# Performance work log

Measured on AMD Instinct MI355X. Metric: run time of the kernel, lower is better.

Reference implementation:

```python
import jax, jax.numpy as jnp
import numpy as np

LN_EPS = 1e-5


def setup_inputs() -> dict:
    key = jax.random.key(0)
    ks = jax.random.split(key, 8)
    B, S, D = 8, 2048, 1024
    scale = 1.0 / np.sqrt(D)
    return {
        "inp": jax.random.normal(ks[0], (B, S, D), dtype=jnp.float32),
        "lens": jax.random.randint(ks[1], (B,), 1, S + 1, dtype=jnp.int64),
        "Wq": jax.random.normal(ks[2], (D, D), dtype=jnp.float32) * scale,
        "bq": jnp.zeros((D,), dtype=jnp.float32),
        "Wk": jax.random.normal(ks[3], (D, D), dtype=jnp.float32) * scale,
        "bk": jnp.zeros((D,), dtype=jnp.float32),
        "Wv": jax.random.normal(ks[4], (D, D), dtype=jnp.float32) * scale,
        "bv": jnp.zeros((D,), dtype=jnp.float32),
        "ln_gamma": jnp.ones((D,), dtype=jnp.float32),
        "ln_beta": jnp.zeros((D,), dtype=jnp.float32),
    }


def reference(inp, lens, Wq, bq, Wk, bk, Wv, bv, ln_gamma, ln_beta):
    # inp: [B, S, D]; dk = dv = D
    B, S, D = inp.shape
    q = jnp.einsum("bsd,kd->bsk", inp, Wq) + bq  # [B, S, D]
    k = jnp.einsum("bsd,kd->bsk", inp, Wk) + bk
    v = jnp.einsum("bsd,kd->bsk", inp, Wv) + bv
    # scores[b, i, j] = q[b, i] . k[b, j]
    scores = jnp.einsum("bid,bjd->bij", q, k)  # [B, S, S]
    # NON-standard: softmax over the QUERY axis (dim=1), then divide by sqrt(dk)
    attn = jax.nn.softmax(scores, axis=1) / jnp.sqrt(jnp.asarray(D, scores.dtype))
    selfatt = jnp.einsum("bij,bjd->bid", attn, v)  # [B, S, D]
    # LayerNorm over last dim, then mean-pool over sequence (sum / seq_len)
    mu = jnp.mean(selfatt, axis=-1, keepdims=True)
    var = jnp.mean(jnp.square(selfatt - mu), axis=-1, keepdims=True)
    ln = (selfatt - mu) * jax.lax.rsqrt(var + LN_EPS) * ln_gamma + ln_beta
    context = jnp.sum(ln, axis=1) / S  # [B, D]
    return context
```

## Files before the change

### kernel.cpp

```cpp
#include <hip/hip_runtime.h>
#include <hip/hip_fp16.h>

#define B_ 8
#define S_ 2048
#define D_ 1024
#define M_ (B_ * S_)
#define NCH 8
#define LN_EPS 1e-5f

typedef _Float16 f16;
typedef _Float16 half8 __attribute__((ext_vector_type(8)));
typedef _Float16 half4_t __attribute__((ext_vector_type(4)));
typedef float floatx4 __attribute__((ext_vector_type(4)));

__device__ __forceinline__ void gload_lds16(const void* g, void* l) {
  __builtin_amdgcn_global_load_lds((const __attribute__((address_space(1))) void*)g,
                                   (__attribute__((address_space(3))) void*)l, 16, 0, 0);
}

__device__ __forceinline__ void xcd_remap(int& bx, int& by, int& bz) {
  const int gx = gridDim.x, gy = gridDim.y;
  const int nb = gx * gy * (int)gridDim.z;
  int f = blockIdx.x + gx * (blockIdx.y + gy * blockIdx.z);
  const int cpx = nb >> 3;
  f = (f & 7) * cpx + (f >> 3);
  bx = f % gx;
  f /= gx;
  by = f % gy;
  bz = f / gy;
}

__global__ void k_cvt(const float* __restrict__ src, f16* __restrict__ dst, int n4) {
  int stride = gridDim.x * blockDim.x;
  for (int i = blockIdx.x * blockDim.x + threadIdx.x; i < n4; i += stride) {
    float4 v = ((const float4*)src)[i];
    half4_t h;
    h.x = (f16)v.x; h.y = (f16)v.y; h.z = (f16)v.z; h.w = (f16)v.w;
    ((half4_t*)dst)[i] = h;
  }
}

__global__ void k_cvtw(const float* __restrict__ a, const float* __restrict__ b,
                       const float* __restrict__ c, f16* __restrict__ dst) {
  const int n4 = D_ * D_ / 4;
  const int i = blockIdx.x * 256 + threadIdx.x;
  const int which = i / n4, off = i - which * n4;
  const float* s = which == 0 ? a : (which == 1 ? b : c);
  const float4 v = ((const float4*)s)[off];
  half4_t h;
  h.x = (f16)v.x; h.y = (f16)v.y; h.z = (f16)v.z; h.w = (f16)v.w;
  ((half4_t*)dst)[i] = h;
}

#define STG_A(tn, h, buf)                                                     \
  {                                                                           \
    const f16* g = aG + (size_t)(tn) * 64 + (size_t)(h) * 128 * K;            \
    f16* l = As + (buf) * 16384 + (h) * 8192 + lOff;                          \
    gload_lds16(g, l);                                                        \
    gload_lds16(g + (size_t)64 * K, l + 4096);                                \
  }
#define STG_B(tn, h, buf)                                                     \
  {                                                                           \
    const f16* g = bG + (size_t)(tn) * 64 + (size_t)(h) * 128 * K;            \
    f16* l = Bs + (buf) * 16384 + (h) * 8192 + lOff;                          \
    gload_lds16(g, l);                                                        \
    gload_lds16(g + (size_t)64 * K, l + 4096);                                \
  }

__device__ __forceinline__ void gemm8_loop(
    const f16* aG, const f16* bG, f16* As, f16* Bs, const int K, const int lOff,
    const int wr, const int wc, const int fr, const int fs0, const int fs1,
    floatx4 (&acc)[2][4][2][2]) {
  const int NT = K >> 6;
  const int NP = NT >> 1;

  STG_A(0, 0, 0);
  STG_B(0, 0, 0);
  STG_B(0, 1, 0);
  STG_A(0, 1, 0);
  STG_A(1, 0, 1);
  STG_B(1, 0, 1);
  asm volatile("s_waitcnt vmcnt(4)" ::: "memory");
  __builtin_amdgcn_s_barrier();

  half8 af[4][2], bf0[2][2], bf1[2][2];

#define LDA(BUF, MH)                                                          \
  _Pragma("unroll") for (int m = 0; m < 4; ++m) {                             \
    const f16* Ac = As + (BUF) * 16384;                                       \
    const int ar = ((MH) * 128 + wr * 64 + m * 16 + fr) * 64;                 \
    af[m][0] = *(const half8*)(Ac + ar + fs0);                                \
    af[m][1] = *(const half8*)(Ac + ar + fs1);                                \
  }
#define LDB(BUF, NH, DST)                                                     \
  _Pragma("unroll") for (int n = 0; n < 2; ++n) {                             \
    const f16* Bc = Bs + (BUF) * 16384;                                       \
    const int br = ((NH) * 128 + wc * 32 + n * 16 + fr) * 64;                 \
    DST[n][0] = *(const half8*)(Bc + br + fs0);                               \
    DST[n][1] = *(const half8*)(Bc + br + fs1);                               \
  }
#define PH(LOADS, MH, NH, BF, STAGE_STMT, WAIT_STMT)                          \
  {                                                                           \
    LOADS;                                                                    \
    STAGE_STMT;                                                               \
    __builtin_amdgcn_s_barrier();                                             \
    __builtin_amdgcn_s_setprio(1);                                            \
    _Pragma("unroll") for (int m = 0; m < 4; ++m)                             \
      _Pragma("unroll") for (int n = 0; n < 2; ++n)                           \
        _Pragma("unroll") for (int kk = 0; kk < 2; ++kk)                      \
          acc[MH][m][NH][n] = __builtin_amdgcn_mfma_f32_16x16x32_f16(         \
              af[m][kk], BF[n][kk], acc[MH][m][NH][n], 0, 0, 0);              \
    __builtin_amdgcn_s_setprio(0);                                            \
    WAIT_STMT;                                                                \
    __builtin_amdgcn_s_barrier();                                             \
  }
#define VW4 asm volatile("s_waitcnt vmcnt(4)" ::: "memory")
#define VW2 asm volatile("s_waitcnt vmcnt(2)" ::: "memory")
#define VW0 asm volatile("s_waitcnt vmcnt(0)" ::: "memory")
#define NOW (void)0

  for (int p = 0; p < NP; ++p) {
    const int t0 = 2 * p;
    const bool mid = (t0 + 2 < NT);
    const bool nxt = (t0 + 3 < NT);
    const bool last = (p == NP - 1);

    PH(LDA(0, 0); LDB(0, 0, bf0), 0, 0, bf0, STG_B(t0 + 1, 1, 1), NOW);
    PH(LDB(0, 1, bf1), 0, 1, bf1, STG_A(t0 + 1, 1, 1), NOW);
    PH(LDA(0, 1), 1, 1, bf1, if (mid) STG_A(t0 + 2, 0, 0), NOW);
    PH(NOW, 1, 0, bf0, if (mid) STG_B(t0 + 2, 0, 0), VW4);
    PH(LDA(1, 0); LDB(1, 0, bf0), 0, 0, bf0, if (mid) STG_B(t0 + 2, 1, 0),
       if (last) { VW2; });
    PH(LDB(1, 1, bf1), 0, 1, bf1, if (mid) STG_A(t0 + 2, 1, 0),
       if (last) { VW0; });
    PH(LDA(1, 1), 1, 1, bf1, if (nxt) STG_A(t0 + 3, 0, 1), NOW);
    PH(NOW, 1, 0, bf0, if (nxt) STG_B(t0 + 3, 0, 1), if (!last) { VW4; });
  }
#undef PH
#undef LDA
#undef LDB
#undef VW4
#undef VW2
#undef VW0
#undef NOW
}

template <bool OUTF16, bool BIAS>
__global__ __launch_bounds__(512, 2) void k_gemm8(
    const f16* __restrict__ A, const f16* __restrict__ Bm, void* __restrict__ Cv,
    const float* __restrict__ bias, const int K, const int N,
    const long sA, const long sB, const long sC) {
  __shared__ f16 As[2 * 256 * 64];
  __shared__ f16 Bs[2 * 256 * 64];
  int bx, by, bz;
  xcd_remap(bx, by, bz);
  const int tid = threadIdx.x;
  const int wid = tid >> 6, lane = tid & 63;
  const int wr = wid >> 2, wc = wid & 3;
  const int fr = lane & 15;

  const f16* Ab = A + (size_t)bz * sA + (size_t)by * 256 * K;
  const f16* Bb = Bm + (size_t)bz * sB + (size_t)bx * 256 * K;
  const int srow = tid >> 3;
  const int sslot = (tid & 7) ^ (srow & 7);
  const f16* aG = Ab + (size_t)srow * K + sslot * 8;
  const f16* bG = Bb + (size_t)srow * K + sslot * 8;
  const int lOff = srow * 64 + (tid & 7) * 8;

  const int sx = lane & 7;
  const int fs0 = (((lane >> 4)) ^ sx) * 8;
  const int fs1 = ((4 + (lane >> 4)) ^ sx) * 8;

  floatx4 acc[2][4][2][2] = {};
  gemm8_loop(aG, bG, As, Bs, K, lOff, wr, wc, fr, fs0, fs1, acc);

#pragma unroll
  for (int mh = 0; mh < 2; ++mh)
#pragma unroll
    for (int m = 0; m < 4; ++m) {
      const int row0 = by * 256 + mh * 128 + wr * 64 + m * 16 + (lane >> 4) * 4;
#pragma unroll
      for (int nh = 0; nh < 2; ++nh)
#pragma unroll
        for (int n = 0; n < 2; ++n) {
          const int col = bx * 256 + nh * 128 + wc * 32 + n * 16 + (lane & 15);
          float bv = 0.0f;
          if constexpr (BIAS) bv = bias[col];
#pragma unroll
          for (int r = 0; r < 4; ++r) {
            const float v = acc[mh][m][nh][n][r] + bv;
            if constexpr (OUTF16)
              ((f16*)Cv)[(size_t)bz * sC + (size_t)(row0 + r) * N + col] = (f16)v;
            else
              ((float*)Cv)[(size_t)bz * sC + (size_t)(row0 + r) * N + col] = v;
          }
        }
    }
}

__global__ __launch_bounds__(512, 2) void k_qkv8b(
    const f16* __restrict__ X, const f16* __restrict__ W,
    f16* __restrict__ Qh, f16* __restrict__ Kh, f16* __restrict__ Vh,
    const float* __restrict__ bq, const float* __restrict__ bk,
    const float* __restrict__ bv) {
  __shared__ f16 As[2 * 256 * 64];
  __shared__ f16 Bs[2 * 256 * 64];
  int bx, by, bz;
  xcd_remap(bx, by, bz);
  const int K = D_;
  const int tid = threadIdx.x;
  const int wid = tid >> 6, lane = tid & 63;
  const int wr = wid >> 2, wc = wid & 3;
  const int fr = lane & 15;

  f16* outp = bz == 0 ? Qh : (bz == 1 ? Kh : Vh);
  const float* bp = bz == 0 ? bq : (bz == 1 ? bk : bv);

  const f16* Ab = X + (size_t)by * 256 * K;
  const f16* Bb = W + (size_t)bz * D_ * D_ + (size_t)bx * 256 * K;
  const int srow = tid >> 3;
  const int sslot = (tid & 7) ^ (srow & 7);
  const f16* aG = Ab + (size_t)srow * K + sslot * 8;
  const f16* bG = Bb + (size_t)srow * K + sslot * 8;
  const int lOff = srow * 64 + (tid & 7) * 8;

  const int sx = lane & 7;
  const int fs0 = (((lane >> 4)) ^ sx) * 8;
  const int fs1 = ((4 + (lane >> 4)) ^ sx) * 8;

  floatx4 acc[2][4][2][2] = {};
  gemm8_loop(aG, bG, As, Bs, K, lOff, wr, wc, fr, fs0, fs1, acc);

#pragma unroll
  for (int mh = 0; mh < 2; ++mh)
#pragma unroll
    for (int m = 0; m < 4; ++m) {
      const int row0 = by * 256 + mh * 128 + wr * 64 + m * 16 + (lane >> 4) * 4;
#pragma unroll
      for (int nh = 0; nh < 2; ++nh)
#pragma unroll
        for (int n = 0; n < 2; ++n) {
          const int col = bx * 256 + nh * 128 + wc * 32 + n * 16 + (lane & 15);
          const float bvv = bp[col];
#pragma unroll
          for (int r = 0; r < 4; ++r)
            outp[(size_t)(row0 + r) * D_ + col] = (f16)(acc[mh][m][nh][n][r] + bvv);
        }
    }
}

__global__ __launch_bounds__(512, 2) void k_scores8(
    const f16* __restrict__ Q, const f16* __restrict__ Kx, f16* __restrict__ Sc,
    float* __restrict__ pm, float* __restrict__ pz) {
  __shared__ f16 As[2 * 256 * 64];
  __shared__ f16 Bs[2 * 256 * 64];
  __shared__ float smax[2][256];
  __shared__ float ssum[2][256];
  int bx, by, bz;
  xcd_remap(bx, by, bz);
  const int tid = threadIdx.x;
  const int wid = tid >> 6, lane = tid & 63;
  const int wr = wid >> 2, wc = wid & 3;
  const int fr = lane & 15;
  const int K = D_;

  const f16* Ab = Q + (size_t)bz * S_ * D_ + (size_t)by * 256 * K;
  const f16* Bb = Kx + (size_t)bz * S_ * D_ + (size_t)bx * 256 * K;
  const int srow = tid >> 3;
  const int sslot = (tid & 7) ^ (srow & 7);
  const f16* aG = Ab + (size_t)srow * K + sslot * 8;
  const f16* bG = Bb + (size_t)srow * K + sslot * 8;
  const int lOff = srow * 64 + (tid & 7) * 8;

  const int sx = lane & 7;
  const int fs0 = (((lane >> 4)) ^ sx) * 8;
  const int fs1 = ((4 + (lane >> 4)) ^ sx) * 8;

  floatx4 acc[2][4][2][2] = {};
  gemm8_loop(aG, bG, As, Bs, K, lOff, wr, wc, fr, fs0, fs1, acc);

#pragma unroll
  for (int mh = 0; mh < 2; ++mh)
#pragma unroll
    for (int m = 0; m < 4; ++m) {
      const int row0 = by * 256 + mh * 128 + wr * 64 + m * 16 + (lane >> 4) * 4;
#pragma unroll
      for (int nh = 0; nh < 2; ++nh)
#pragma unroll
        for (int n = 0; n < 2; ++n) {
          const int col = bx * 256 + nh * 128 + wc * 32 + n * 16 + fr;
#pragma unroll
          for (int r = 0; r < 4; ++r)
            Sc[(size_t)bz * S_ * S_ + (size_t)(row0 + r) * S_ + col] =
                (f16)acc[mh][m][nh][n][r];
        }
    }

  float cmax[2][2], csum[2][2];
#pragma unroll
  for (int nh = 0; nh < 2; ++nh)
#pragma unroll
    for (int n = 0; n < 2; ++n) {
      float mx = -1e30f;
#pragma unroll
      for (int mh = 0; mh < 2; ++mh)
#pragma unroll
        for (int m = 0; m < 4; ++m)
#pragma unroll
          for (int r = 0; r < 4; ++r)
            mx = fmaxf(mx, (float)(f16)acc[mh][m][nh][n][r]);
      float zz = 0.f;
#pragma unroll
      for (int mh = 0; mh < 2; ++mh)
#pragma unroll
        for (int m = 0; m < 4; ++m)
#pragma unroll
          for (int r = 0; r < 4; ++r)
            zz += __expf((float)(f16)acc[mh][m][nh][n][r] - mx);
#pragma unroll
      for (int o = 16; o <= 32; o <<= 1) {
        const float om = __shfl_xor(mx, o);
        const float oz = __shfl_xor(zz, o);
        const float nm = fmaxf(mx, om);
        zz = zz * __expf(mx - nm) + oz * __expf(om - nm);
        mx = nm;
      }
      cmax[nh][n] = mx;
      csum[nh][n] = zz;
    }
  __syncthreads();
  if ((lane >> 4) == 0) {
#pragma unroll
    for (int nh = 0; nh < 2; ++nh)
#pragma unroll
      for (int n = 0; n < 2; ++n) {
        const int c = nh * 128 + wc * 32 + n * 16 + fr;
        smax[wr][c] = cmax[nh][n];
        ssum[wr][c] = csum[nh][n];
      }
  }
  __syncthreads();
  if (wr == 0 && (lane >> 4) == 0) {
#pragma unroll
    for (int nh = 0; nh < 2; ++nh)
#pragma unroll
      for (int n = 0; n < 2; ++n) {
        const int c = nh * 128 + wc * 32 + n * 16 + fr;
        const float m0 = smax[0][c], m1 = smax[1][c];
        const float nm = fmaxf(m0, m1);
        const float zz = ssum[0][c] * __expf(m0 - nm) + ssum[1][c] * __expf(m1 - nm);
        const size_t o = ((size_t)bz * NCH + by) * S_ + bx * 256 + c;
        pm[o] = nm;
        pz[o] = zz;
      }
  }
}

__global__ void k_combine(const float* __restrict__ pm, const float* __restrict__ pz,
                          float* __restrict__ mcol, float* __restrict__ cscale) {
  const int b = blockIdx.y;
  const int j = blockIdx.x * 256 + threadIdx.x;
  float m = -1e30f;
#pragma unroll
  for (int ch = 0; ch < NCH; ++ch) m = fmaxf(m, pm[((size_t)b * NCH + ch) * S_ + j]);
  float z = 0.f;
#pragma unroll
  for (int ch = 0; ch < NCH; ++ch)
    z += pz[((size_t)b * NCH + ch) * S_ + j] * __expf(pm[((size_t)b * NCH + ch) * S_ + j] - m);
  mcol[(size_t)b * S_ + j] = m;
  cscale[(size_t)b * S_ + j] = 1.0f / (z * 32.0f);
}

__global__ void k_pexp16(f16* __restrict__ P, const float* __restrict__ mcol,
                         const float* __restrict__ cscale) {
  const int n4 = B_ * S_ * S_ / 4;
  const int stride = gridDim.x * blockDim.x;
  for (int i = blockIdx.x * blockDim.x + threadIdx.x; i < n4; i += stride) {
    const size_t e = (size_t)i * 4;
    const int z = (int)(e / ((size_t)S_ * S_));
    const int j = (int)(e & (S_ - 1));
    const half4_t s4 = ((const half4_t*)P)[i];
    const float4 mv = *(const float4*)(mcol + (size_t)z * S_ + j);
    const float4 cv = *(const float4*)(cscale + (size_t)z * S_ + j);
    half4_t h;
    h.x = (f16)(__expf((float)s4.x - mv.x) * cv.x);
    h.y = (f16)(__expf((float)s4.y - mv.y) * cv.y);
    h.z = (f16)(__expf((float)s4.z - mv.z) * cv.z);
    h.w = (f16)(__expf((float)s4.w - mv.w) * cv.w);
    ((half4_t*)P)[i] = h;
  }
}

__global__ void k_transpose(const f16* __restrict__ V, f16* __restrict__ Vt) {
  __shared__ f16 t[64][72];
  const int b = blockIdx.z;
  const int j0 = blockIdx.x * 64, d0 = blockIdx.y * 64;
  const int rr = threadIdx.x >> 4;
  const int cc = (threadIdx.x & 15) * 4;
#pragma unroll
  for (int p = 0; p < 4; ++p) {
    const int j = rr + p * 16;
    const half4_t v = *(const half4_t*)(V + ((size_t)b * S_ + j0 + j) * D_ + d0 + cc);
    *(half4_t*)&t[j][cc] = v;
  }
  __syncthreads();
#pragma unroll
  for (int p = 0; p < 4; ++p) {
    const int d = rr + p * 16;
    half4_t v;
    v.x = t[cc][d]; v.y = t[cc + 1][d]; v.z = t[cc + 2][d]; v.w = t[cc + 3][d];
    *(half4_t*)(Vt + ((size_t)b * D_ + d0 + d) * S_ + j0 + cc) = v;
  }
}

__global__ __launch_bounds__(256) void k_ln_pool(
    const f16* __restrict__ selfatt, const float* __restrict__ gamma,
    const float* __restrict__ beta, float* __restrict__ part) {
  __shared__ float lds[4 * 1024];
  const int tid = threadIdx.x, wid = tid >> 6, lane = tid & 63;
  const int row0 = blockIdx.x * 64 + wid * 16;
  float g[16], be[16], acc[16];
#pragma unroll
  for (int t = 0; t < 16; ++t) {
    g[t] = gamma[lane + 64 * t];
    be[t] = beta[lane + 64 * t];
    acc[t] = 0.f;
  }
  for (int r = 0; r < 16; ++r) {
    const f16* xp = selfatt + (size_t)(row0 + r) * D_ + lane;
    float x[16], sum = 0.f, sq = 0.f;
#pragma unroll
    for (int t = 0; t < 16; ++t) {
      x[t] = (float)xp[64 * t];
      sum += x[t];
      sq += x[t] * x[t];
    }
#pragma unroll
    for (int o = 32; o > 0; o >>= 1) {
      sum += __shfl_xor(sum, o);
      sq += __shfl_xor(sq, o);
    }
    const float mu = sum * (1.f / 1024.f);
    const float var = sq * (1.f / 1024.f) - mu * mu;
    const float rstd = rsqrtf(var + LN_EPS);
#pragma unroll
    for (int t = 0; t < 16; ++t) acc[t] += (x[t] - mu) * rstd * g[t] + be[t];
  }
#pragma unroll
  for (int t = 0; t < 16; ++t) lds[wid * 1024 + lane + 64 * t] = acc[t];
  __syncthreads();
#pragma unroll
  for (int c = 0; c < 4; ++c) {
    const int d = tid + 256 * c;
    const float s = lds[d] + lds[1024 + d] + lds[2048 + d] + lds[3072 + d];
    part[(size_t)blockIdx.x * 1024 + d] = s;
  }
}

__global__ void k_final(const float* __restrict__ part, float* __restrict__ out) {
  const int idx = blockIdx.x * 256 + threadIdx.x;
  const int b = idx >> 10, d = idx & 1023;
  float s = 0.f;
#pragma unroll
  for (int slot = 0; slot < 32; ++slot)
    s += part[((size_t)(b * 32 + slot)) * 1024 + d];
  out[idx] = s * (1.0f / S_);
}

extern "C" void kernel_launch(void* const* d_in, const int* in_sizes, int n_in,
                              void* d_out, int out_size, void* d_ws, size_t ws_size,
                              hipStream_t stream) {
  (void)in_sizes; (void)n_in; (void)out_size;
  const float* inp = (const float*)d_in[0];
  const float* Wq = (const float*)d_in[2];
  const float* bq = (const float*)d_in[3];
  const float* Wk = (const float*)d_in[4];
  const float* bk = (const float*)d_in[5];
  const float* Wv = (const float*)d_in[6];
  const float* bv = (const float*)d_in[7];
  const float* gamma = (const float*)d_in[8];
  const float* beta = (const float*)d_in[9];
  float* out = (float*)d_out;

  char* ws = (char*)d_ws;
  const size_t MB = 1024 * 1024;
  if (ws_size < 244 * MB) return;

  f16* Xh = (f16*)(ws);
  f16* Qh = (f16*)(ws + 32 * MB);
  f16* Kh = (f16*)(ws + 64 * MB);
  f16* Vh = (f16*)(ws + 96 * MB);
  f16* Vt = (f16*)(ws + 128 * MB);
  f16* Sc = (f16*)(ws + 160 * MB);
  f16* Wh = (f16*)(ws + 224 * MB);
  float* pm = (float*)(ws + 230 * MB);
  float* pz = (float*)(ws + 231 * MB);
  float* mcol = (float*)(ws + 232 * MB);
  float* cscale = mcol + (size_t)B_ * S_;
  float* part = (float*)(ws + 233 * MB);
  f16* selfatt = Xh;

  k_cvt<<<2048, 256, 0, stream>>>(inp, Xh, M_ * D_ / 4);
  k_cvtw<<<3 * D_ * D_ / 4 / 256, 256, 0, stream>>>(Wq, Wk, Wv, Wh);

  k_qkv8b<<<dim3(D_ / 256, M_ / 256, 3), 512, 0, stream>>>(
      Xh, Wh, Qh, Kh, Vh, bq, bk, bv);

  k_transpose<<<dim3(S_ / 64, D_ / 64, B_), 256, 0, stream>>>(Vh, Vt);

  k_scores8<<<dim3(S_ / 256, S_ / 256, B_), 512, 0, stream>>>(Qh, Kh, Sc, pm, pz);
  k_combine<<<dim3(S_ / 256, B_), 256, 0, stream>>>(pm, pz, mcol, cscale);
  k_pexp16<<<2048, 256, 0, stream>>>(Sc, mcol, cscale);

  k_gemm8<true, false><<<dim3(D_ / 256, S_ / 256, B_), 512, 0, stream>>>(
      Sc, Vt, selfatt, nullptr, S_, D_,
      (long)S_ * S_, (long)D_ * S_, (long)S_ * D_);

  k_ln_pool<<<M_ / 64, 256, 0, stream>>>(selfatt, gamma, beta, part);
  k_final<<<(B_ * D_) / 256, 256, 0, stream>>>(part, out);
}
```

Before: 315.1 us.

## Fuse column-softmax exponent into scores epilogue and rescale in PV GEMM

The scores kernel now writes exp(score minus the block-local column max) directly in its epilogue, instead of writing raw scores that a separate elementwise pass later re-reads and rewrites. The per-chunk correction factor (global max and normalizer) is computed in k_combine as an f16 table. The new PV GEMM loads it into LDS and multiplies each A fragment by it before the MFMA. This removes one full read and write pass over the B×S×S f16 score matrix. In exchange the GEMM inner loop gains vector multiplies on A fragments plus an extra LDS load, and storing unnormalized exponentials and scale factors in f16 may cost some precision.

```diff
diff --git a/kernel.cpp b/kernel.cpp
--- a/kernel.cpp
+++ b/kernel.cpp
@@ -67,10 +67,11 @@
     gload_lds16(g + (size_t)64 * K, l + 4096);                                \
   }
 
+template <bool SCL>
 __device__ __forceinline__ void gemm8_loop(
-    const f16* aG, const f16* bG, f16* As, f16* Bs, const int K, const int lOff,
-    const int wr, const int wc, const int fr, const int fs0, const int fs1,
-    floatx4 (&acc)[2][4][2][2]) {
+    const f16* aG, const f16* bG, f16* As, f16* Bs, const f16* Ss,
+    const int K, const int lOff, const int wr, const int wc, const int fr,
+    const int lg, const int fs0, const int fs1, floatx4 (&acc)[2][4][2][2]) {
   const int NT = K >> 6;
   const int NP = NT >> 1;
 
@@ -84,13 +85,25 @@
   __builtin_amdgcn_s_barrier();
 
   half8 af[4][2], bf0[2][2], bf1[2][2];
-
+  half8 sclv0 = {}, sclv1 = {};
+  (void)lg;
+
+#define LDSCL(T)                                                              \
+  if constexpr (SCL) {                                                        \
+    const f16* sp = Ss + (T) * 64 + lg * 8;                                   \
+    sclv0 = *(const half8*)sp;                                                \
+    sclv1 = *(const half8*)(sp + 32);                                         \
+  }
 #define LDA(BUF, MH)                                                          \
   _Pragma("unroll") for (int m = 0; m < 4; ++m) {                             \
     const f16* Ac = As + (BUF) * 16384;                                       \
     const int ar = ((MH) * 128 + wr * 64 + m * 16 + fr) * 64;                 \
     af[m][0] = *(const half8*)(Ac + ar + fs0);                                \
     af[m][1] = *(const half8*)(Ac + ar + fs1);                                \
+    if constexpr (SCL) {                                                      \
+      af[m][0] = af[m][0] * sclv0;                                            \
+      af[m][1] = af[m][1] * sclv1;                                            \
+    }                                                                         \
   }
 #define LDB(BUF, NH, DST)                                                     \
   _Pragma("unroll") for (int n = 0; n < 2; ++n) {                             \
@@ -125,12 +138,12 @@
     const bool nxt = (t0 + 3 < NT);
     const bool last = (p == NP - 1);
 
-    PH(LDA(0, 0); LDB(0, 0, bf0), 0, 0, bf0, STG_B(t0 + 1, 1, 1), NOW);
+    PH(LDSCL(t0); LDA(0, 0); LDB(0, 0, bf0), 0, 0, bf0, STG_B(t0 + 1, 1, 1), NOW);
     PH(LDB(0, 1, bf1), 0, 1, bf1, STG_A(t0 + 1, 1, 1), NOW);
     PH(LDA(0, 1), 1, 1, bf1, if (mid) STG_A(t0 + 2, 0, 0), NOW);
     PH(NOW, 1, 0, bf0, if (mid) STG_B(t0 + 2, 0, 0), VW4);
-    PH(LDA(1, 0); LDB(1, 0, bf0), 0, 0, bf0, if (mid) STG_B(t0 + 2, 1, 0),
-       if (last) { VW2; });
+    PH(LDSCL(t0 + 1); LDA(1, 0); LDB(1, 0, bf0), 0, 0, bf0,
+       if (mid) STG_B(t0 + 2, 1, 0), if (last) { VW2; });
     PH(LDB(1, 1, bf1), 0, 1, bf1, if (mid) STG_A(t0 + 2, 1, 0),
        if (last) { VW0; });
     PH(LDA(1, 1), 1, 1, bf1, if (nxt) STG_A(t0 + 3, 0, 1), NOW);
@@ -139,63 +152,11 @@
 #undef PH
 #undef LDA
 #undef LDB
+#undef LDSCL
 #undef VW4
 #undef VW2
 #undef VW0
 #undef NOW
-}
-
-template <bool OUTF16, bool BIAS>
-__global__ __launch_bounds__(512, 2) void k_gemm8(
-    const f16* __restrict__ A, const f16* __restrict__ Bm, void* __restrict__ Cv,
-    const float* __restrict__ bias, const int K, const int N,
-    const long sA, const long sB, const long sC) {
-  __shared__ f16 As[2 * 256 * 64];
-  __shared__ f16 Bs[2 * 256 * 64];
-  int bx, by, bz;
-  xcd_remap(bx, by, bz);
-  const int tid = threadIdx.x;
-  const int wid = tid >> 6, lane = tid & 63;
-  const int wr = wid >> 2, wc = wid & 3;
-  const int fr = lane & 15;
-
-  const f16* Ab = A + (size_t)bz * sA + (size_t)by * 256 * K;
-  const f16* Bb = Bm + (size_t)bz * sB + (size_t)bx * 256 * K;
-  const int srow = tid >> 3;
-  const int sslot = (tid & 7) ^ (srow & 7);
-  const f16* aG = Ab + (size_t)srow * K + sslot * 8;
-  const f16* bG = Bb + (size_t)srow * K + sslot * 8;
-  const int lOff = srow * 64 + (tid & 7) * 8;
-
-  const int sx = lane & 7;
-  const int fs0 = (((lane >> 4)) ^ sx) * 8;
-  const int fs1 = ((4 + (lane >> 4)) ^ sx) * 8;
-
-  floatx4 acc[2][4][2][2] = {};
-  gemm8_loop(aG, bG, As, Bs, K, lOff, wr, wc, fr, fs0, fs1, acc);
-
-#pragma unroll
-  for (int mh = 0; mh < 2; ++mh)
-#pragma unroll
-    for (int m = 0; m < 4; ++m) {
-      const int row0 = by * 256 + mh * 128 + wr * 64 + m * 16 + (lane >> 4) * 4;
-#pragma unroll
-      for (int nh = 0; nh < 2; ++nh)
-#pragma unroll
-        for (int n = 0; n < 2; ++n) {
-          const int col = bx * 256 + nh * 128 + wc * 32 + n * 16 + (lane & 15);
-          float bv = 0.0f;
-          if constexpr (BIAS) bv = bias[col];
-#pragma unroll
-          for (int r = 0; r < 4; ++r) {
-            const float v = acc[mh][m][nh][n][r] + bv;
-            if constexpr (OUTF16)
-              ((f16*)Cv)[(size_t)bz * sC + (size_t)(row0 + r) * N + col] = (f16)v;
-            else
-              ((float*)Cv)[(size_t)bz * sC + (size_t)(row0 + r) * N + col] = v;
-          }
-        }
-    }
 }
 
 __global__ __launch_bounds__(512, 2) void k_qkv8b(
@@ -211,7 +172,7 @@
   const int tid = threadIdx.x;
   const int wid = tid >> 6, lane = tid & 63;
   const int wr = wid >> 2, wc = wid & 3;
-  const int fr = lane & 15;
+  const int fr = lane & 15, lg = lane >> 4;
 
   f16* outp = bz == 0 ? Qh : (bz == 1 ? Kh : Vh);
   const float* bp = bz == 0 ? bq : (bz == 1 ? bk : bv);
@@ -225,11 +186,11 @@
   const int lOff = srow * 64 + (tid & 7) * 8;
 
   const int sx = lane & 7;
-  const int fs0 = (((lane >> 4)) ^ sx) * 8;
-  const int fs1 = ((4 + (lane >> 4)) ^ sx) * 8;
+  const int fs0 = ((lg) ^ sx) * 8;
+  const int fs1 = ((4 + lg) ^ sx) * 8;
 
   floatx4 acc[2][4][2][2] = {};
-  gemm8_loop(aG, bG, As, Bs, K, lOff, wr, wc, fr, fs0, fs1, acc);
+  gemm8_loop<false>(aG, bG, As, Bs, nullptr, K, lOff, wr, wc, fr, lg, fs0, fs1, acc);
 
 #pragma unroll
   for (int mh = 0; mh < 2; ++mh)
@@ -261,7 +222,7 @@
   const int tid = threadIdx.x;
   const int wid = tid >> 6, lane = tid & 63;
   const int wr = wid >> 2, wc = wid & 3;
-  const int fr = lane & 15;
+  const int fr = lane & 15, lg = lane >> 4;
   const int K = D_;
 
   const f16* Ab = Q + (size_t)bz * S_ * D_ + (size_t)by * 256 * K;
@@ -273,28 +234,11 @@
   const int lOff = srow * 64 + (tid & 7) * 8;
 
   const int sx = lane & 7;
-  const int fs0 = (((lane >> 4)) ^ sx) * 8;
-  const int fs1 = ((4 + (lane >> 4)) ^ sx) * 8;
+  const int fs0 = ((lg) ^ sx) * 8;
+  const int fs1 = ((4 + lg) ^ sx) * 8;
 
   floatx4 acc[2][4][2][2] = {};
-  gemm8_loop(aG, bG, As, Bs, K, lOff, wr, wc, fr, fs0, fs1, acc);
-
-#pragma unroll
-  for (int mh = 0; mh < 2; ++mh)
-#pragma unroll
-    for (int m = 0; m < 4; ++m) {
-      const int row0 = by * 256 + mh * 128 + wr * 64 + m * 16 + (lane >> 4) * 4;
-#pragma unroll
-      for (int nh = 0; nh < 2; ++nh)
-#pragma unroll
-        for (int n = 0; n < 2; ++n) {
-          const int col = bx * 256 + nh * 128 + wc * 32 + n * 16 + fr;
-#pragma unroll
-          for (int r = 0; r < 4; ++r)
-            Sc[(size_t)bz * S_ * S_ + (size_t)(row0 + r) * S_ + col] =
-                (f16)acc[mh][m][nh][n][r];
-        }
-    }
+  gemm8_loop<false>(aG, bG, As, Bs, nullptr, K, lOff, wr, wc, fr, lg, fs0, fs1, acc);
 
   float cmax[2][2], csum[2][2];
 #pragma unroll
@@ -329,7 +273,7 @@
       csum[nh][n] = zz;
     }
   __syncthreads();
-  if ((lane >> 4) == 0) {
+  if (lg == 0) {
 #pragma unroll
     for (int nh = 0; nh < 2; ++nh)
 #pragma unroll
@@ -340,7 +284,34 @@
       }
   }
   __syncthreads();
-  if (wr == 0 && (lane >> 4) == 0) {
+
+  float mt[2][2];
+#pragma unroll
+  for (int nh = 0; nh < 2; ++nh)
+#pragma unroll
+    for (int n = 0; n < 2; ++n) {
+      const int c = nh * 128 + wc * 32 + n * 16 + fr;
+      mt[nh][n] = fmaxf(smax[0][c], smax[1][c]);
+    }
+
+#pragma unroll
+  for (int mh = 0; mh < 2; ++mh)
+#pragma unroll
+    for (int m = 0; m < 4; ++m) {
+      const int row0 = by * 256 + mh * 128 + wr * 64 + m * 16 + (lane >> 4) * 4;
+#pragma unroll
+      for (int nh = 0; nh < 2; ++nh)
+#pragma unroll
+        for (int n = 0; n < 2; ++n) {
+          const int col = bx * 256 + nh * 128 + wc * 32 + n * 16 + fr;
+#pragma unroll
+          for (int r = 0; r < 4; ++r)
+            Sc[(size_t)bz * S_ * S_ + (size_t)(row0 + r) * S_ + col] =
+                (f16)__expf((float)(f16)acc[mh][m][nh][n][r] - mt[nh][n]);
+        }
+    }
+
+  if (wr == 0 && lg == 0) {
 #pragma unroll
     for (int nh = 0; nh < 2; ++nh)
 #pragma unroll
@@ -357,7 +328,7 @@
 }
 
 __global__ void k_combine(const float* __restrict__ pm, const float* __restrict__ pz,
-                          float* __restrict__ mcol, float* __restrict__ cscale) {
+                          f16* __restrict__ sclh) {
   const int b = blockIdx.y;
   const int j = blockIdx.x * 256 + threadIdx.x;
   float m = -1e30f;
@@ -367,28 +338,61 @@
 #pragma unroll
   for (int ch = 0; ch < NCH; ++ch)
     z += pz[((size_t)b * NCH + ch) * S_ + j] * __expf(pm[((size_t)b * NCH + ch) * S_ + j] - m);
-  mcol[(size_t)b * S_ + j] = m;
-  cscale[(size_t)b * S_ + j] = 1.0f / (z * 32.0f);
-}
-
-__global__ void k_pexp16(f16* __restrict__ P, const float* __restrict__ mcol,
-                         const float* __restrict__ cscale) {
-  const int n4 = B_ * S_ * S_ / 4;
-  const int stride = gridDim.x * blockDim.x;
-  for (int i = blockIdx.x * blockDim.x + threadIdx.x; i < n4; i += stride) {
-    const size_t e = (size_t)i * 4;
-    const int z = (int)(e / ((size_t)S_ * S_));
-    const int j = (int)(e & (S_ - 1));
-    const half4_t s4 = ((const half4_t*)P)[i];
-    const float4 mv = *(const float4*)(mcol + (size_t)z * S_ + j);
-    const float4 cv = *(const float4*)(cscale + (size_t)z * S_ + j);
-    half4_t h;
-    h.x = (f16)(__expf((float)s4.x - mv.x) * cv.x);
-    h.y = (f16)(__expf((float)s4.y - mv.y) * cv.y);
-    h.z = (f16)(__expf((float)s4.z - mv.z) * cv.z);
-    h.w = (f16)(__expf((float)s4.w - mv.w) * cv.w);
-    ((half4_t*)P)[i] = h;
-  }
+  const float csc = 1.0f / (z * 32.0f);
+#pragma unroll
+  for (int ch = 0; ch < NCH; ++ch)
+    sclh[((size_t)ch * B_ + b) * S_ + j] =
+        (f16)(__expf(pm[((size_t)b * NCH + ch) * S_ + j] - m) * csc);
+}
+
+__global__ __launch_bounds__(512, 2) void k_pv8(
+    const f16* __restrict__ P, const f16* __restrict__ Vt,
+    const f16* __restrict__ sclh, f16* __restrict__ selfatt) {
+  __shared__ f16 As[2 * 256 * 64];
+  __shared__ f16 Bs[2 * 256 * 64];
+  __shared__ f16 Ss[2048];
+  int bx, by, bz;
+  xcd_remap(bx, by, bz);
+  const int K = S_;
+  const int tid = threadIdx.x;
+  const int wid = tid >> 6, lane = tid & 63;
+  const int wr = wid >> 2, wc = wid & 3;
+  const int fr = lane & 15, lg = lane >> 4;
+
+  const f16* Ab = P + (size_t)bz * S_ * S_ + (size_t)by * 256 * K;
+  const f16* Bb = Vt + (size_t)bz * D_ * S_ + (size_t)bx * 256 * K;
+  const int srow = tid >> 3;
+  const int sslot = (tid & 7) ^ (srow & 7);
+  const f16* aG = Ab + (size_t)srow * K + sslot * 8;
+  const f16* bG = Bb + (size_t)srow * K + sslot * 8;
+  const int lOff = srow * 64 + (tid & 7) * 8;
+
+  const int sx = lane & 7;
+  const int fs0 = ((lg) ^ sx) * 8;
+  const int fs1 = ((4 + lg) ^ sx) * 8;
+
+  if (tid < 256)
+    gload_lds16(sclh + ((size_t)by * B_ + bz) * S_ + tid * 8, Ss + tid * 8);
+
+  floatx4 acc[2][4][2][2] = {};
+  gemm8_loop<true>(aG, bG, As, Bs, Ss, K, lOff, wr, wc, fr, lg, fs0, fs1, acc);
+
+#pragma unroll
+  for (int mh = 0; mh < 2; ++mh)
+#pragma unroll
+    for (int m = 0; m < 4; ++m) {
+      const int row0 = by * 256 + mh * 128 + wr * 64 + m * 16 + (lane >> 4) * 4;
+#pragma unroll
+      for (int nh = 0; nh < 2; ++nh)
+#pragma unroll
+        for (int n = 0; n < 2; ++n) {
+          const int col = bx * 256 + nh * 128 + wc * 32 + n * 16 + (lane & 15);
+#pragma unroll
+          for (int r = 0; r < 4; ++r)
+            selfatt[(size_t)(bz * S_ + row0 + r) * D_ + col] =
+                (f16)acc[mh][m][nh][n][r];
+        }
+    }
 }
 
 __global__ void k_transpose(const f16* __restrict__ V, f16* __restrict__ Vt) {
@@ -495,8 +499,7 @@
   f16* Wh = (f16*)(ws + 224 * MB);
   float* pm = (float*)(ws + 230 * MB);
   float* pz = (float*)(ws + 231 * MB);
-  float* mcol = (float*)(ws + 232 * MB);
-  float* cscale = mcol + (size_t)B_ * S_;
+  f16* sclh = (f16*)(ws + 232 * MB);
   float* part = (float*)(ws + 233 * MB);
   f16* selfatt = Xh;
 
@@ -509,12 +512,9 @@
   k_transpose<<<dim3(S_ / 64, D_ / 64, B_), 256, 0, stream>>>(Vh, Vt);
 
   k_scores8<<<dim3(S_ / 256, S_ / 256, B_), 512, 0, stream>>>(Qh, Kh, Sc, pm, pz);
-  k_combine<<<dim3(S_ / 256, B_), 256, 0, stream>>>(pm, pz, mcol, cscale);
-  k_pexp16<<<2048, 256, 0, stream>>>(Sc, mcol, cscale);
-
-  k_gemm8<true, false><<<dim3(D_ / 256, S_ / 256, B_), 512, 0, stream>>>(
-      Sc, Vt, selfatt, nullptr, S_, D_,
-      (long)S_ * S_, (long)D_ * S_, (long)S_ * D_);
+  k_combine<<<dim3(S_ / 256, B_), 256, 0, stream>>>(pm, pz, sclh);
+
+  k_pv8<<<dim3(D_ / 256, S_ / 256, B_), 512, 0, stream>>>(Sc, Vt, sclh, selfatt);
 
   k_ln_pool<<<M_ / 64, 256, 0, stream>>>(selfatt, gamma, beta, part);
   k_final<<<(B_ * D_) / 256, 256, 0, stream>>>(part, out);
```

Result: faster. 298.1 us (-5.4%).
